# Kernel optimization log

Measured on AMD Instinct MI355X. Metric: run time of the kernel, lower is better.

## Reference

```python
import jax, jax.numpy as jnp
import numpy as np

# Config constants (match init_kwargs)
D_MODEL = 1024
N_EXPERTS = 8
EXPERT_SCALE = 2          # experts per base group -> n_base_groups = 4
N_FEAT = 16
BANK_DIM = 32
RAW_FEAT = N_FEAT * BANK_DIM   # 512
PROJ_DIM = 256
R_HIDDEN = 256
E_HIDDEN = 256
TOP_K = 2
TEMP = 1.0
LN_EPS = 1e-5


def _layernorm(x, g, b):
    mu = jnp.mean(x, axis=-1, keepdims=True)
    var = jnp.mean((x - mu) ** 2, axis=-1, keepdims=True)
    return (x - mu) * jax.lax.rsqrt(var + LN_EPS) * g + b


def _softmax_top_k(logits, k):
    # keep top-k logits, mask rest to -inf, softmax
    topv = jax.lax.top_k(logits, k)[0]
    thresh = topv[..., -1:]
    masked = jnp.where(logits >= thresh, logits, -jnp.inf)
    return jax.nn.softmax(masked, axis=-1)


def setup_inputs() -> dict:
    key = jax.random.key(0)
    ks = jax.random.split(key, 24)
    B, S = 4, 2048
    s = 0.02
    inp = {
        "hidden": jax.random.normal(ks[0], (B, S, D_MODEL), jnp.float32),
        "feat": jax.random.normal(ks[1], (B, S, N_FEAT), jnp.float32),
        "feat_bank": jax.random.normal(ks[2], (B, S, N_FEAT, BANK_DIM), jnp.float32),
        "item_seq_len": jax.random.randint(ks[3], (B,), 1, S + 1, jnp.int64),
        # pre-LN
        "ln_g": jnp.ones((D_MODEL,), jnp.float32),
        "ln_b": jnp.zeros((D_MODEL,), jnp.float32),
        # router feature projector (2 layers: Linear -> GELU -> Linear)
        "fp_w1": jax.random.normal(ks[4], (RAW_FEAT, PROJ_DIM), jnp.float32) * s,
        "fp_b1": jnp.zeros((PROJ_DIM,), jnp.float32),
        "fp_w2": jax.random.normal(ks[5], (PROJ_DIM, PROJ_DIM), jnp.float32) * s,
        "fp_b2": jnp.zeros((PROJ_DIM,), jnp.float32),
        # learned router MLP: d_in = d_model + proj_dim
        "r_w1": jax.random.normal(ks[6], (D_MODEL + PROJ_DIM, R_HIDDEN), jnp.float32) * s,
        "r_b1": jnp.zeros((R_HIDDEN,), jnp.float32),
        "r_w2": jax.random.normal(ks[7], (R_HIDDEN, N_EXPERTS), jnp.float32) * s,
        "r_b2": jnp.zeros((N_EXPERTS,), jnp.float32),
        # rule router (linear on raw stage features)
        "rr_w": jax.random.normal(ks[8], (N_FEAT, N_EXPERTS), jnp.float32) * s,
        "rr_b": jnp.zeros((N_EXPERTS,), jnp.float32),
        # per-expert FFN
        "e_w1": jax.random.normal(ks[9], (N_EXPERTS, D_MODEL, E_HIDDEN), jnp.float32) * s,
        "e_b1": jnp.zeros((N_EXPERTS, E_HIDDEN), jnp.float32),
        "e_w2": jax.random.normal(ks[10], (N_EXPERTS, E_HIDDEN, D_MODEL), jnp.float32) * s,
        "e_b2": jnp.zeros((N_EXPERTS, D_MODEL), jnp.float32),
        "alpha": jnp.ones((), jnp.float32),
    }
    return inp


def reference(hidden, feat, feat_bank, item_seq_len, ln_g, ln_b,
              fp_w1, fp_b1, fp_w2, fp_b2,
              r_w1, r_b1, r_w2, r_b2,
              rr_w, rr_b,
              e_w1, e_b1, e_w2, e_b2, alpha):
    B, S, D = hidden.shape
    h_norm = _layernorm(hidden, ln_g, ln_b)  # [B,S,D]

    # router feature path: flatten bank, 2-layer GELU projector
    bank_flat = feat_bank.reshape(B, S, RAW_FEAT)
    proj = jnp.dot(jax.nn.gelu(jnp.dot(bank_flat, fp_w1) + fp_b1), fp_w2) + fp_b2  # [B,S,P]

    # token-mode router input: concat hidden + projected features
    router_input = jnp.concatenate([h_norm, proj], axis=-1)
    rule_logits = jnp.dot(feat, rr_w) + rr_b  # rule router on raw stage features

    raw_logits = jnp.dot(jax.nn.gelu(jnp.dot(router_input, r_w1) + r_b1), r_w2) + r_b2
    scaled_logits = raw_logits / max(TEMP, 1e-6)
    gate_weights = _softmax_top_k(scaled_logits, TOP_K)           # [B,S,E]
    rule_target_logits = rule_logits / max(TEMP, 1e-6)

    # expert group: per-expert 2-layer GELU FFN on h_norm
    h1 = jax.nn.gelu(jnp.einsum('bsd,edh->bseh', h_norm, e_w1) + e_b1)
    expert_out = jnp.einsum('bseh,ehd->bsed', h1, e_w2) + e_b2    # [B,S,E,D]

    stage_out = jnp.einsum('bse,bsed->bsd', gate_weights, expert_out)
    next_hidden = hidden + alpha * stage_out

    # _aggregate_group_weights: expert_group_idx = arange(E)//EXPERT_SCALE is
    # contiguous, so gather+sum per group == reshape+sum over the scale axis
    n_groups = N_EXPERTS // EXPERT_SCALE
    group_weights = gate_weights.reshape(B, S, n_groups, EXPERT_SCALE).sum(-1)

    return (next_hidden, stage_out, gate_weights, scaled_logits, group_weights, rule_target_logits)
```

## Files before the change

### kernel.cpp

```cpp
#include <hip/hip_runtime.h>
#include <stdint.h>


typedef unsigned short u16;
using bf16x8 = __attribute__((ext_vector_type(8))) short;
using f32x4  = __attribute__((ext_vector_type(4))) float;

#define WS_HHI 0u
#define WS_HLO 16777216u
#define WS_PB2 33554432u
#define WS_W1T 67108864u
#define WS_IDX 71303168u
#define IX_SELE   0u
#define IX_SELG   65536u
#define IX_ROW    131072u
#define IX_TOKR   196608u
#define IX_GROW   262144u
#define IX_CNT    327680u
#define IX_CBASE  335872u
#define IX_TILEE  344064u
#define IX_TILES  344704u
#define IX_TILEC  345344u
#define IX_META   345984u
#define IX_TILEE2 346112u
#define IX_TILES2 347264u
#define IX_TILEC2 348416u

__device__ __forceinline__ float gelu_tanh(float x) {
  float x3 = x * x * x;
  float t = tanhf(0.7978845608028654f * (x + 0.044715f * x3));
  return 0.5f * x * (1.0f + t);
}
__device__ __forceinline__ u16 f2bf(float f) {
  uint32_t u = __float_as_uint(f);
  u = u + 0x7fffu + ((u >> 16) & 1u);
  return (u16)(u >> 16);
}
__device__ __forceinline__ float b2f(u16 h) {
  return __uint_as_float(((uint32_t)h) << 16);
}
__device__ __forceinline__ void gll16(const void* g, void* l) {
  __builtin_amdgcn_global_load_lds(
      (const __attribute__((address_space(1))) void*)g,
      (__attribute__((address_space(3))) void*)l, 16, 0, 0);
}

__global__ __launch_bounds__(256) void split_bank_kernel(const float* __restrict__ x,
    u16* __restrict__ hi, u16* __restrict__ lo) {
  int i4 = blockIdx.x * 256 + threadIdx.x;
  float4 v = ((const float4*)x)[i4];
  ushort4 h, l;
  h.x = f2bf(v.x); l.x = f2bf(v.x - b2f(h.x));
  h.y = f2bf(v.y); l.y = f2bf(v.y - b2f(h.y));
  h.z = f2bf(v.z); l.z = f2bf(v.z - b2f(h.z));
  h.w = f2bf(v.w); l.w = f2bf(v.w - b2f(h.w));
  ((ushort4*)hi)[i4] = h;
  ((ushort4*)lo)[i4] = l;
}

__global__ __launch_bounds__(256) void tsplit_kernel(const float* __restrict__ in,
    int inR, int inC, u16* __restrict__ outHi, u16* __restrict__ outLo,
    int outLD, int outColOff) {
  __shared__ u16 hs[64][65];
  __shared__ u16 ls[64][65];
  int tid = threadIdx.x;
  int c0 = blockIdx.x * 64, r0 = blockIdx.y * 64;
  const float* inp = in + (size_t)blockIdx.z * inR * inC;
  int rl = tid >> 6, cl = tid & 63;
#pragma unroll
  for (int p = 0; p < 16; p++) {
    int r = rl + p * 4;
    float v = inp[(size_t)(r0 + r) * inC + c0 + cl];
    u16 h = f2bf(v);
    hs[r][cl] = h;
    ls[r][cl] = f2bf(v - b2f(h));
  }
  __syncthreads();
  size_t obase = (size_t)(blockIdx.z * inC + c0) * outLD + outColOff + r0;
#pragma unroll
  for (int p = 0; p < 16; p++) {
    int c = rl + p * 4;
    outHi[obase + (size_t)c * outLD + cl] = hs[cl][c];
    if (outLo) outLo[obase + (size_t)c * outLD + cl] = ls[cl][c];
  }
}

__global__ __launch_bounds__(256) void wprime_kernel(const float* __restrict__ fp_w2,
    const float* __restrict__ r_w1, const float* __restrict__ fp_b2,
    const float* __restrict__ r_b1, float* __restrict__ wp, float* __restrict__ bp) {
  __shared__ float row[256];
  int i = blockIdx.x, n = threadIdx.x;
  if (i < 256) {
    row[n] = fp_w2[i * 256 + n];
    __syncthreads();
    float acc = 0.0f;
    for (int j = 0; j < 256; j++) acc += row[j] * r_w1[(size_t)(1024 + j) * 256 + n];
    wp[i * 256 + n] = acc;
  } else {
    row[n] = fp_b2[n];
    __syncthreads();
    float acc = r_b1[n];
    for (int j = 0; j < 256; j++) acc += row[j] * r_w1[(size_t)(1024 + j) * 256 + n];
    bp[n] = acc;
  }
}

__global__ __launch_bounds__(256) void ln_kernel(const float* __restrict__ hidden,
    const float* __restrict__ ln_g, const float* __restrict__ ln_b,
    const float* __restrict__ feat, const float* __restrict__ rr_w,
    const float* __restrict__ rr_b,
    u16* __restrict__ h_hi, u16* __restrict__ h_lo, float* __restrict__ rule) {
  int t = blockIdx.x;
  int tid = threadIdx.x;
  float4 v = ((const float4*)(hidden + (size_t)t * 1024))[tid];
  float s = v.x + v.y + v.z + v.w;
#pragma unroll
  for (int o = 32; o > 0; o >>= 1) s += __shfl_down(s, o);
  __shared__ float red[4];
  __shared__ float stats[2];
  int wid = tid >> 6, lane = tid & 63;
  if (lane == 0) red[wid] = s;
  __syncthreads();
  if (tid == 0) stats[0] = (red[0] + red[1] + red[2] + red[3]) * (1.0f / 1024.0f);
  __syncthreads();
  float mu = stats[0];
  float dx = v.x - mu, dy = v.y - mu, dz = v.z - mu, dw = v.w - mu;
  float q = dx * dx + dy * dy + dz * dz + dw * dw;
#pragma unroll
  for (int o = 32; o > 0; o >>= 1) q += __shfl_down(q, o);
  if (lane == 0) red[wid] = q;
  __syncthreads();
  if (tid == 0) {
    float var = (red[0] + red[1] + red[2] + red[3]) * (1.0f / 1024.0f) + 1e-5f;
    float r = rsqrtf(var);
    r = r * (1.5f - 0.5f * var * r * r);
    stats[1] = r;
  }
  __syncthreads();
  float r = stats[1];
  float4 g = ((const float4*)ln_g)[tid];
  float4 b = ((const float4*)ln_b)[tid];
  float4 o;
  o.x = dx * r * g.x + b.x;
  o.y = dy * r * g.y + b.y;
  o.z = dz * r * g.z + b.z;
  o.w = dw * r * g.w + b.w;
  ushort4 hv, lv;
  hv.x = f2bf(o.x); lv.x = f2bf(o.x - b2f(hv.x));
  hv.y = f2bf(o.y); lv.y = f2bf(o.y - b2f(hv.y));
  hv.z = f2bf(o.z); lv.z = f2bf(o.z - b2f(hv.z));
  hv.w = f2bf(o.w); lv.w = f2bf(o.w - b2f(hv.w));
  ((ushort4*)(h_hi + (size_t)t * 1024))[tid] = hv;
  ((ushort4*)(h_lo + (size_t)t * 1024))[tid] = lv;
  if (tid < 8) {
    float acc = rr_b[tid];
#pragma unroll
    for (int f = 0; f < 16; f++) acc += feat[t * 16 + f] * rr_w[f * 8 + tid];
    rule[t * 8 + tid] = acc;
  }
}

#define G3_STAGE(K, AH, AL, BH, BL)   \
  gll16(gAh0 + (K), AH + tid * 8);    \
  gll16(gAl0 + (K), AL + tid * 8);    \
  gll16(gBh0 + (K), BH + tid * 8);    \
  gll16(gBl0 + (K), BL + tid * 8);

#define G3_COMPUTE(AH, AL, BH, BL)                                             \
  {                                                                            \
    bf16x8 afh[2], afl[2], bfh[2], bfl[2];                                     \
    _Pragma("unroll") for (int i = 0; i < 2; i++) {                            \
      afh[i] = *((const bf16x8*)(AH + (wr + i * 16 + l16) * 32 + xq * 8));     \
      afl[i] = *((const bf16x8*)(AL + (wr + i * 16 + l16) * 32 + xq * 8));     \
      bfh[i] = *((const bf16x8*)(BH + (wc + i * 16 + l16) * 32 + xq * 8));     \
      bfl[i] = *((const bf16x8*)(BL + (wc + i * 16 + l16) * 32 + xq * 8));     \
    }                                                                          \
    _Pragma("unroll") for (int i = 0; i < 2; i++)                              \
      _Pragma("unroll") for (int j = 0; j < 2; j++) {                          \
        acc[i][j] = __builtin_amdgcn_mfma_f32_16x16x32_bf16(afh[i], bfh[j], acc[i][j], 0, 0, 0); \
        acc[i][j] = __builtin_amdgcn_mfma_f32_16x16x32_bf16(afl[i], bfh[j], acc[i][j], 0, 0, 0); \
        acc[i][j] = __builtin_amdgcn_mfma_f32_16x16x32_bf16(afh[i], bfl[j], acc[i][j], 0, 0, 0); \
      }                                                                        \
  }

__global__ __launch_bounds__(256) void gemm3_kernel(
    const u16* __restrict__ Ah, const u16* __restrict__ Al, int lda,
    int kchunk, int nz1,
    const u16* __restrict__ A2h, const u16* __restrict__ A2l, int lda2,
    int klen2, int bkoff2,
    const u16* __restrict__ Bth, const u16* __restrict__ Btl, int Kb,
    float* __restrict__ parts) {
  __shared__ u16 Ash0[2048], Ash1[2048];
  __shared__ u16 Asl0[2048], Asl1[2048];
  __shared__ u16 Bsh0[2048], Bsh1[2048];
  __shared__ u16 Bsl0[2048], Bsl1[2048];
  int tid = threadIdx.x;
  int z = blockIdx.z;
  const u16 *pAh, *pAl;
  int lda_, akoff, bkoff, klen;
  if (z < nz1) {
    pAh = Ah; pAl = Al; lda_ = lda; akoff = z * kchunk; bkoff = akoff; klen = kchunk;
  } else {
    pAh = A2h; pAl = A2l; lda_ = lda2; akoff = 0; bkoff = bkoff2; klen = klen2;
  }
  int row0 = blockIdx.y * 64, col0 = blockIdx.x * 64;
  int wave = tid >> 6, lane = tid & 63;
  int wr = (wave >> 1) * 32, wc = (wave & 1) * 32;
  int l16 = lane & 15, qd = lane >> 4;
  int xq = qd ^ ((l16 >> 1) & 3);
  f32x4 acc[2][2];
#pragma unroll
  for (int i = 0; i < 2; i++)
#pragma unroll
    for (int j = 0; j < 2; j++) acc[i][j] = 0.0f;

  int r0 = tid >> 2, kc = tid & 3;
  int kcs = kc ^ ((r0 >> 1) & 3);
  const u16* gAh0 = pAh + (size_t)(row0 + r0) * lda_ + akoff + kcs * 8;
  const u16* gAl0 = pAl + (size_t)(row0 + r0) * lda_ + akoff + kcs * 8;
  const u16* gBh0 = Bth + (size_t)(col0 + r0) * Kb + bkoff + kcs * 8;
  const u16* gBl0 = Btl + (size_t)(col0 + r0) * Kb + bkoff + kcs * 8;

  G3_STAGE(0, Ash0, Asl0, Bsh0, Bsl0);
  __syncthreads();
  for (int k0 = 0; k0 < klen; k0 += 64) {
    G3_STAGE(k0 + 32, Ash1, Asl1, Bsh1, Bsl1);
    G3_COMPUTE(Ash0, Asl0, Bsh0, Bsl0);
    __syncthreads();
    if (k0 + 64 < klen) {
      G3_STAGE(k0 + 64, Ash0, Asl0, Bsh0, Bsl0);
    }
    G3_COMPUTE(Ash1, Asl1, Bsh1, Bsl1);
    __syncthreads();
  }

  float* pz = parts + (size_t)z * 2097152;
#pragma unroll
  for (int i = 0; i < 2; i++)
#pragma unroll
    for (int j = 0; j < 2; j++) {
      int cl = wc + j * 16 + l16;
#pragma unroll
      for (int rr = 0; rr < 4; rr++) {
        int rl = wr + i * 16 + qd * 4 + rr;
        pz[(size_t)(row0 + rl) * 256 + col0 + cl] = acc[i][j][rr];
      }
    }
}

__global__ __launch_bounds__(256) void epi_bf_kernel(const float* __restrict__ parts,
    int nz, const float* __restrict__ bias, int do_gelu,
    u16* __restrict__ hi, u16* __restrict__ lo) {
  int i4 = blockIdx.x * 256 + threadIdx.x;
  float4 s = ((const float4*)parts)[i4];
  for (int zz = 1; zz < nz; zz++) {
    float4 p = ((const float4*)parts)[(size_t)zz * 524288 + i4];
    s.x += p.x; s.y += p.y; s.z += p.z; s.w += p.w;
  }
  float4 bv = ((const float4*)bias)[i4 & 63];
  s.x += bv.x; s.y += bv.y; s.z += bv.z; s.w += bv.w;
  if (do_gelu) {
    s.x = gelu_tanh(s.x); s.y = gelu_tanh(s.y);
    s.z = gelu_tanh(s.z); s.w = gelu_tanh(s.w);
  }
  ushort4 h, l;
  h.x = f2bf(s.x); l.x = f2bf(s.x - b2f(h.x));
  h.y = f2bf(s.y); l.y = f2bf(s.y - b2f(h.y));
  h.z = f2bf(s.z); l.z = f2bf(s.z - b2f(h.z));
  h.w = f2bf(s.w); l.w = f2bf(s.w - b2f(h.w));
  ((ushort4*)hi)[i4] = h;
  ((ushort4*)lo)[i4] = l;
}

__global__ __launch_bounds__(256) void epi_f32_kernel(const float* __restrict__ parts,
    int nz, const float* __restrict__ bias, float* __restrict__ out) {
  int i4 = blockIdx.x * 256 + threadIdx.x;
  float4 s = ((const float4*)parts)[i4];
  for (int zz = 1; zz < nz; zz++) {
    float4 p = ((const float4*)parts)[(size_t)zz * 524288 + i4];
    s.x += p.x; s.y += p.y; s.z += p.z; s.w += p.w;
  }
  float4 bv = ((const float4*)bias)[i4 & 63];
  s.x = gelu_tanh(s.x + bv.x);
  s.y = gelu_tanh(s.y + bv.y);
  s.z = gelu_tanh(s.z + bv.z);
  s.w = gelu_tanh(s.w + bv.w);
  ((float4*)out)[i4] = s;
}

__global__ __launch_bounds__(256) void gate_kernel(const float* __restrict__ r1,
    const float* __restrict__ r_w2, const float* __restrict__ r_b2,
    float* __restrict__ gates, float* __restrict__ slog, float* __restrict__ gw,
    int* __restrict__ selE, float* __restrict__ selG, int* __restrict__ cnt) {
  __shared__ float w2s[2048];
  __shared__ float r1s[32][260];
  __shared__ float lg[32][8];
  __shared__ int se_s[64];
  int tid = threadIdx.x;
  int blk = blockIdx.x;
  int t0 = blk * 32;
  for (int i = tid; i < 2048; i += 256) {
    int e = i >> 8, k = i & 255;
    w2s[i] = r_w2[k * 8 + e];
  }
  for (int i = tid; i < 8192; i += 256) {
    int tt = i >> 8, k = i & 255;
    r1s[tt][k] = r1[(size_t)(t0 + tt) * 256 + k];
  }
  __syncthreads();
  {
    int tl = tid >> 3, e = tid & 7;
    float acc = r_b2[e];
    const float* wrp = &w2s[e * 256];
    const float* rrp = &r1s[tl][0];
    for (int k = 0; k < 256; k += 4) {
      float4 a = *(const float4*)(rrp + k);
      float4 b = *(const float4*)(wrp + k);
      acc += a.x * b.x + a.y * b.y + a.z * b.z + a.w * b.w;
    }
    lg[tl][e] = acc;
  }
  __syncthreads();
  if (tid < 32) {
    int t = t0 + tid;
    float l[8];
#pragma unroll
    for (int i = 0; i < 8; i++) l[i] = lg[tid][i];
    float m1 = -1e30f, m2 = -1e30f;
    int i1 = 0, i2 = 0;
#pragma unroll
    for (int i = 0; i < 8; i++) {
      float v = l[i];
      if (v > m1) { m2 = m1; i2 = i1; m1 = v; i1 = i; }
      else if (v > m2) { m2 = v; i2 = i; }
    }
    float w[8];
    float se = 0.0f;
#pragma unroll
    for (int i = 0; i < 8; i++) {
      float ex = (l[i] >= m2) ? expf(l[i] - m1) : 0.0f;
      w[i] = ex;
      se += ex;
    }
    float inv = 1.0f / se;
#pragma unroll
    for (int i = 0; i < 8; i++) {
      gates[(size_t)t * 8 + i] = w[i] * inv;
      slog[(size_t)t * 8 + i] = l[i];
    }
#pragma unroll
    for (int gi = 0; gi < 4; gi++)
      gw[(size_t)t * 4 + gi] = (w[2 * gi] + w[2 * gi + 1]) * inv;
    se_s[tid * 2] = i1;
    se_s[tid * 2 + 1] = i2;
    selE[t * 2] = i1;      selG[t * 2] = w[i1] * inv;
    selE[t * 2 + 1] = i2;  selG[t * 2 + 1] = w[i2] * inv;
  }
  __syncthreads();
  if (tid < 8) {
    int c = 0;
#pragma unroll
    for (int s = 0; s < 64; s++) c += (se_s[s] == tid) ? 1 : 0;
    cnt[blk * 8 + tid] = c;
  }
}

__global__ __launch_bounds__(256) void stageb_kernel(const int* __restrict__ cnt,
    int* __restrict__ cbase, int* __restrict__ tileE, int* __restrict__ tileS,
    int* __restrict__ tileC, int* __restrict__ tileE2, int* __restrict__ tileS2,
    int* __restrict__ tileC2, int* __restrict__ meta) {
  __shared__ int cs[2048];
  __shared__ int tot[8];
  __shared__ int ebase[8];
  int tid = threadIdx.x;
  for (int i = tid; i < 2048; i += 256) cs[i] = cnt[i];
  __syncthreads();
  if (tid < 8) {
    int s = 0;
    for (int c = 0; c < 256; c++) s += cs[c * 8 + tid];
    tot[tid] = s;
  }
  __syncthreads();
  if (tid == 0) {
    int b = 0, nt = 0;
    for (int e = 0; e < 8; e++) {
      ebase[e] = b;
      int c = tot[e];
      for (int off = 0; off < c; off += 128) {
        tileE[nt] = e; tileS[nt] = b + off;
        tileC[nt] = (c - off < 128) ? (c - off) : 128;
        nt++;
      }
      b += c;
    }
    meta[16] = nt;
    int b2 = 0, nt2 = 0;
    for (int e = 0; e < 8; e++) {
      int c = tot[e];
      for (int off = 0; off < c; off += 64) {
        tileE2[nt2] = e; tileS2[nt2] = b2 + off;
        tileC2[nt2] = (c - off < 64) ? (c - off) : 64;
        nt2++;
      }
      b2 += c;
    }
    meta[17] = nt2;
  }
  __syncthreads();
  if (tid < 8) {
    int run = ebase[tid];
    for (int c = 0; c < 256; c++) {
      cbase[c * 8 + tid] = run;
      run += cs[c * 8 + tid];
    }
  }
}

__global__ __launch_bounds__(256) void scatter_kernel(const int* __restrict__ selE,
    const float* __restrict__ selG, const int* __restrict__ cbase,
    int* __restrict__ rowsel, int* __restrict__ tokrow, float* __restrict__ grow) {
  int chunk = blockIdx.x;
  int wave = threadIdx.x >> 6, lane = threadIdx.x & 63;
  int slot = chunk * 64 + lane;
  int sel = selE[slot];
  float g = selG[slot];
  int tokn = chunk * 32 + (lane >> 1);
  unsigned long long lt = (1ULL << lane) - 1ULL;
#pragma unroll
  for (int ei = 0; ei < 2; ei++) {
    int e = wave + ei * 4;
    unsigned long long m = __ballot(sel == e);
    if (sel == e) {
      int row = cbase[chunk * 8 + e] + __popcll(m & lt);
      rowsel[slot] = row;
      tokrow[row] = tokn;
      grow[row] = g;
    }
  }
}

__global__ __launch_bounds__(256) void gexp1_kernel(const u16* __restrict__ A,
    const u16* __restrict__ w1t, const float* __restrict__ e_b1,
    const int* __restrict__ tokrow, const float* __restrict__ grow,
    const int* __restrict__ tileE2, const int* __restrict__ tileS2,
    const int* __restrict__ tileC2, const int* __restrict__ meta,
    u16* __restrict__ pb1) {
  __shared__ u16 As0[64 * 32];
  __shared__ u16 As1[64 * 32];
  __shared__ u16 Bs0[64 * 32];
  __shared__ u16 Bs1[64 * 32];
  __shared__ float gsl[64];
  int n = blockIdx.x;
  int ty = ((n >> 5) << 3) + (n & 7);
  int cblk = (n >> 3) & 3;
  if (ty >= meta[17]) return;
  int e = tileE2[ty], pstart = tileS2[ty], pcnt = tileC2[ty];
  int tid = threadIdx.x;
  int col0 = cblk * 64;
  if (tid < 64) {
    int rr = (tid < pcnt) ? tid : (pcnt - 1);
    gsl[tid] = grow[pstart + rr];
  }
  int wave = tid >> 6, lane = tid & 63;
  int wr = (wave >> 1) * 32, wc = (wave & 1) * 32;
  int l16 = lane & 15, qd = lane >> 4;
  int xq = qd ^ ((l16 >> 1) & 3);
  f32x4 acc[2][2];
  acc[0][0] = 0.0f; acc[0][1] = 0.0f; acc[1][0] = 0.0f; acc[1][1] = 0.0f;

  int r0 = tid >> 2, kc = tid & 3;
  int kcs = kc ^ ((r0 >> 1) & 3);
  int ra = (r0 < pcnt) ? r0 : (pcnt - 1);
  int ta = tokrow[pstart + ra];
  const u16* Ap = A + (size_t)ta * 1024 + kcs * 8;
  const u16* Bp = w1t + (size_t)(e * 256 + col0 + r0) * 1024 + kcs * 8;
  u16* dA0 = As0 + tid * 8;
  u16* dA1 = As1 + tid * 8;
  u16* dB0 = Bs0 + tid * 8;
  u16* dB1 = Bs1 + tid * 8;

  int aoff0 = (wr + l16) * 32 + xq * 8;
  int aoff1 = aoff0 + 16 * 32;
  int boff0 = (wc + l16) * 32 + xq * 8;
  int boff1 = boff0 + 16 * 32;

  gll16(Ap, dA0);
  gll16(Bp, dB0);
  __syncthreads();

  for (int k0 = 0; k0 < 1024; k0 += 64) {
    {
      gll16(Ap + k0 + 32, dA1);
      gll16(Bp + k0 + 32, dB1);
      bf16x8 a0 = *((const bf16x8*)(As0 + aoff0));
      bf16x8 a1 = *((const bf16x8*)(As0 + aoff1));
      bf16x8 b0 = *((const bf16x8*)(Bs0 + boff0));
      bf16x8 b1 = *((const bf16x8*)(Bs0 + boff1));
      acc[0][0] = __builtin_amdgcn_mfma_f32_16x16x32_bf16(a0, b0, acc[0][0], 0, 0, 0);
      acc[0][1] = __builtin_amdgcn_mfma_f32_16x16x32_bf16(a0, b1, acc[0][1], 0, 0, 0);
      acc[1][0] = __builtin_amdgcn_mfma_f32_16x16x32_bf16(a1, b0, acc[1][0], 0, 0, 0);
      acc[1][1] = __builtin_amdgcn_mfma_f32_16x16x32_bf16(a1, b1, acc[1][1], 0, 0, 0);
      __syncthreads();
    }
    {
      if (k0 + 64 < 1024) {
        gll16(Ap + k0 + 64, dA0);
        gll16(Bp + k0 + 64, dB0);
      }
      bf16x8 a0 = *((const bf16x8*)(As1 + aoff0));
      bf16x8 a1 = *((const bf16x8*)(As1 + aoff1));
      bf16x8 b0 = *((const bf16x8*)(Bs1 + boff0));
      bf16x8 b1 = *((const bf16x8*)(Bs1 + boff1));
      acc[0][0] = __builtin_amdgcn_mfma_f32_16x16x32_bf16(a0, b0, acc[0][0], 0, 0, 0);
      acc[0][1] = __builtin_amdgcn_mfma_f32_16x16x32_bf16(a0, b1, acc[0][1], 0, 0, 0);
      acc[1][0] = __builtin_amdgcn_mfma_f32_16x16x32_bf16(a1, b0, acc[1][0], 0, 0, 0);
      acc[1][1] = __builtin_amdgcn_mfma_f32_16x16x32_bf16(a1, b1, acc[1][1], 0, 0, 0);
      __syncthreads();
    }
  }

#pragma unroll
  for (int i = 0; i < 2; i++)
#pragma unroll
    for (int j = 0; j < 2; j++) {
      int cl = wc + j * 16 + l16;
      int col = col0 + cl;
      float bc = e_b1[e * 256 + col];
#pragma unroll
      for (int rr = 0; rr < 4; rr++) {
        int rl = wr + i * 16 + qd * 4 + rr;
        if (rl < pcnt) {
          float v = gelu_tanh(acc[i][j][rr] + bc) * gsl[rl];
          pb1[(size_t)(pstart + rl) * 256 + col] = f2bf(v);
        }
      }
    }
}

#define GX2_STAGE(K, AS, BS)              \
  gll16(Ap0 + (K), AS + tid * 8);         \
  gll16(Ap1 + (K), AS + tid * 8 + 2048);  \
  gll16(Bp0 + (K), BS + tid * 8);         \
  gll16(Bp1 + (K), BS + tid * 8 + 2048);

#define GX2_COMPUTE(AS, BS)                                                   \
  {                                                                           \
    bf16x8 af[4], bfr[4];                                                     \
    _Pragma("unroll") for (int i = 0; i < 4; i++) {                           \
      af[i]  = *((const bf16x8*)(AS + (wr + i * 16 + l16) * 32 + xq * 8));    \
      bfr[i] = *((const bf16x8*)(BS + (wc + i * 16 + l16) * 32 + xq * 8));    \
    }                                                                         \
    _Pragma("unroll") for (int i = 0; i < 4; i++)                             \
      _Pragma("unroll") for (int j = 0; j < 4; j++)                           \
        acc[i][j] = __builtin_amdgcn_mfma_f32_16x16x32_bf16(af[i], bfr[j], acc[i][j], 0, 0, 0); \
  }

__global__ __launch_bounds__(256) void gexp2_kernel(const u16* __restrict__ pb1,
    const u16* __restrict__ w2te,
    const int* __restrict__ tileE, const int* __restrict__ tileS,
    const int* __restrict__ tileC, const int* __restrict__ meta,
    u16* __restrict__ pb2) {
  int ty = blockIdx.y;
  if (ty >= meta[16]) return;
  int e = tileE[ty], pstart = tileS[ty], pcnt = tileC[ty];
  if (pcnt <= 0) return;
  __shared__ u16 As0[4096], As1[4096];
  __shared__ u16 Bs0[4096], Bs1[4096];
  int tid = threadIdx.x;
  int col0 = blockIdx.x * 128;
  int wave = tid >> 6, lane = tid & 63;
  int wr = (wave >> 1) * 64, wc = (wave & 1) * 64;
  int l16 = lane & 15, qd = lane >> 4;
  int xq = qd ^ ((l16 >> 1) & 3);
  f32x4 acc[4][4];
#pragma unroll
  for (int i = 0; i < 4; i++)
#pragma unroll
    for (int j = 0; j < 4; j++) acc[i][j] = 0.0f;

  int r0 = tid >> 2, kc = tid & 3;
  int kcs = kc ^ ((r0 >> 1) & 3);
  int ra = (r0 < pcnt) ? r0 : (pcnt - 1);
  int rb = (r0 + 64 < pcnt) ? (r0 + 64) : (pcnt - 1);
  const u16* Ap0 = pb1 + (size_t)(pstart + ra) * 256 + kcs * 8;
  const u16* Ap1 = pb1 + (size_t)(pstart + rb) * 256 + kcs * 8;
  const u16* Bp0 = w2te + (size_t)(e * 1024 + col0 + r0) * 256 + kcs * 8;
  const u16* Bp1 = Bp0 + (size_t)64 * 256;

  GX2_STAGE(0, As0, Bs0);
  __syncthreads();
  for (int k0 = 0; k0 < 256; k0 += 64) {
    GX2_STAGE(k0 + 32, As1, Bs1);
    GX2_COMPUTE(As0, Bs0);
    __syncthreads();
    if (k0 + 64 < 256) {
      GX2_STAGE(k0 + 64, As0, Bs0);
    }
    GX2_COMPUTE(As1, Bs1);
    __syncthreads();
  }

#pragma unroll
  for (int i = 0; i < 4; i++)
#pragma unroll
    for (int j = 0; j < 4; j++) {
      int cl = wc + j * 16 + l16;
#pragma unroll
      for (int rr = 0; rr < 4; rr++) {
        int rl = wr + i * 16 + qd * 4 + rr;
        if (rl < pcnt)
          pb2[(size_t)(pstart + rl) * 1024 + col0 + cl] = f2bf(acc[i][j][rr]);
      }
    }
}

__global__ __launch_bounds__(256) void combine_kernel(const u16* __restrict__ pb2,
    const int* __restrict__ rowsel, const int* __restrict__ selE,
    const float* __restrict__ selG, const float* __restrict__ e_b2,
    const float* __restrict__ hidden, const float* __restrict__ alpha_p,
    float* __restrict__ stage, float* __restrict__ next) {
  int t = blockIdx.x;
  int c = threadIdx.x * 4;
  int rA = rowsel[t * 2], rB = rowsel[t * 2 + 1];
  int eA = selE[t * 2], eB = selE[t * 2 + 1];
  float gA = selG[t * 2], gB = selG[t * 2 + 1];
  float al = alpha_p[0];
  ushort4 pa = *((const ushort4*)(pb2 + (size_t)rA * 1024 + c));
  ushort4 pb = *((const ushort4*)(pb2 + (size_t)rB * 1024 + c));
  float4 ba = *((const float4*)(e_b2 + (size_t)eA * 1024 + c));
  float4 bb = *((const float4*)(e_b2 + (size_t)eB * 1024 + c));
  float4 h = *((const float4*)(hidden + (size_t)t * 1024 + c));
  float4 v;
  v.x = b2f(pa.x) + b2f(pb.x) + gA * ba.x + gB * bb.x;
  v.y = b2f(pa.y) + b2f(pb.y) + gA * ba.y + gB * bb.y;
  v.z = b2f(pa.z) + b2f(pb.z) + gA * ba.z + gB * bb.z;
  v.w = b2f(pa.w) + b2f(pb.w) + gA * ba.w + gB * bb.w;
  *((float4*)(stage + (size_t)t * 1024 + c)) = v;
  float4 n;
  n.x = h.x + al * v.x; n.y = h.y + al * v.y;
  n.z = h.z + al * v.z; n.w = h.w + al * v.w;
  *((float4*)(next + (size_t)t * 1024 + c)) = n;
}

extern "C" void kernel_launch(void* const* d_in, const int* in_sizes, int n_in,
                              void* d_out, int out_size, void* d_ws, size_t ws_size,
                              hipStream_t stream) {
  const float* hidden    = (const float*)d_in[0];
  const float* feat      = (const float*)d_in[1];
  const float* feat_bank = (const float*)d_in[2];
  const float* ln_g  = (const float*)d_in[4];
  const float* ln_b  = (const float*)d_in[5];
  const float* fp_w1 = (const float*)d_in[6];
  const float* fp_b1 = (const float*)d_in[7];
  const float* fp_w2 = (const float*)d_in[8];
  const float* fp_b2 = (const float*)d_in[9];
  const float* r_w1  = (const float*)d_in[10];
  const float* r_b1  = (const float*)d_in[11];
  const float* r_w2  = (const float*)d_in[12];
  const float* r_b2  = (const float*)d_in[13];
  const float* rr_w  = (const float*)d_in[14];
  const float* rr_b  = (const float*)d_in[15];
  const float* e_w1  = (const float*)d_in[16];
  const float* e_b1  = (const float*)d_in[17];
  const float* e_w2  = (const float*)d_in[18];
  const float* e_b2  = (const float*)d_in[19];
  const float* alpha = (const float*)d_in[20];

  char* ob = (char*)d_out;
  float* next  = (float*)ob;
  float* stage = (float*)(ob + 33554432);
  float* gates = (float*)(ob + 67108864);
  float* slog  = gates + 65536;
  float* gw    = slog + 65536;
  float* rule  = gw + 32768;

  u16* bank_hi  = (u16*)ob;
  u16* bank_lo  = (u16*)(ob + 8388608);
  float* r1     = (float*)ob;
  u16* fpw1t_hi = (u16*)(ob + 16777216);
  u16* fpw1t_lo = (u16*)(ob + 17039360);
  float* wp     = (float*)(ob + 17301504);
  float* bp     = (float*)(ob + 17563648);
  u16* rw1t_hi  = (u16*)(ob + 17825792);
  u16* rw1t_lo  = (u16*)(ob + 18481152);
  u16* mid_hi   = (u16*)(ob + 19136512);
  u16* mid_lo   = (u16*)(ob + 23330816);
  u16* w2te     = (u16*)(ob + 19136512);

  char* sb = ob + 33554432;
  float* parts = (float*)sb;
  u16* pb1     = (u16*)sb;

  char* ws = (char*)d_ws;
  u16* h_hi = (u16*)(ws + WS_HHI);
  u16* h_lo = (u16*)(ws + WS_HLO);
  u16* pb2  = (u16*)(ws + WS_PB2);
  u16* w1t  = (u16*)(ws + WS_W1T);
  char* ix  = ws + WS_IDX;
  int*   selE   = (int*)(ix + IX_SELE);
  float* selG   = (float*)(ix + IX_SELG);
  int*   rowsel = (int*)(ix + IX_ROW);
  int*   tokrow = (int*)(ix + IX_TOKR);
  float* grow   = (float*)(ix + IX_GROW);
  int*   cnt    = (int*)(ix + IX_CNT);
  int*   cbase  = (int*)(ix + IX_CBASE);
  int*   tileE  = (int*)(ix + IX_TILEE);
  int*   tileS  = (int*)(ix + IX_TILES);
  int*   tileC  = (int*)(ix + IX_TILEC);
  int*   tileE2 = (int*)(ix + IX_TILEE2);
  int*   tileS2 = (int*)(ix + IX_TILES2);
  int*   tileC2 = (int*)(ix + IX_TILEC2);
  int*   meta   = (int*)(ix + IX_META);

  split_bank_kernel<<<4096, 256, 0, stream>>>(feat_bank, bank_hi, bank_lo);
  wprime_kernel<<<257, 256, 0, stream>>>(fp_w2, r_w1, fp_b2, r_b1, wp, bp);
  tsplit_kernel<<<dim3(4, 8, 1), 256, 0, stream>>>(fp_w1, 512, 256,
      fpw1t_hi, fpw1t_lo, 512, 0);
  tsplit_kernel<<<dim3(4, 16, 1), 256, 0, stream>>>(r_w1, 1024, 256,
      rw1t_hi, rw1t_lo, 1280, 0);
  tsplit_kernel<<<dim3(4, 4, 1), 256, 0, stream>>>(wp, 256, 256,
      rw1t_hi, rw1t_lo, 1280, 1024);
  tsplit_kernel<<<dim3(4, 16, 8), 256, 0, stream>>>(e_w1, 1024, 256,
      w1t, nullptr, 1024, 0);
  ln_kernel<<<8192, 256, 0, stream>>>(hidden, ln_g, ln_b, feat, rr_w, rr_b,
                                      h_hi, h_lo, rule);
  gemm3_kernel<<<dim3(4, 128, 2), 256, 0, stream>>>(
      bank_hi, bank_lo, 512, 256, 2,
      bank_hi, bank_lo, 512, 0, 0,
      fpw1t_hi, fpw1t_lo, 512, parts);
  epi_bf_kernel<<<2048, 256, 0, stream>>>(parts, 2, fp_b1, 1, mid_hi, mid_lo);
  gemm3_kernel<<<dim3(4, 128, 3), 256, 0, stream>>>(
      h_hi, h_lo, 1024, 512, 2,
      mid_hi, mid_lo, 256, 256, 1024,
      rw1t_hi, rw1t_lo, 1280, parts);
  tsplit_kernel<<<dim3(16, 4, 8), 256, 0, stream>>>(e_w2, 256, 1024,
      w2te, nullptr, 256, 0);
  epi_f32_kernel<<<2048, 256, 0, stream>>>(parts, 3, bp, r1);
  gate_kernel<<<256, 256, 0, stream>>>(r1, r_w2, r_b2, gates, slog, gw,
      selE, selG, cnt);
  stageb_kernel<<<1, 256, 0, stream>>>(cnt, cbase, tileE, tileS, tileC,
      tileE2, tileS2, tileC2, meta);
  scatter_kernel<<<256, 256, 0, stream>>>(selE, selG, cbase, rowsel, tokrow, grow);
  gexp1_kernel<<<1152, 256, 0, stream>>>(h_hi, w1t, e_b1, tokrow, grow,
      tileE2, tileS2, tileC2, meta, pb1);
  gexp2_kernel<<<dim3(8, 136), 256, 0, stream>>>(pb1, w2te, tileE, tileS, tileC,
      meta, pb2);
  combine_kernel<<<8192, 256, 0, stream>>>(pb2, rowsel, selE, selG, e_b2,
      hidden, alpha, stage, next);
}
```

Measured before the change: 359.7 us.

## Fuse router GEMMs with bias-GELU epilogues and drop split-K partials

Replaces the split-K GEMM plus separate reduction/epilogue kernels with one kernel per router GEMM that walks the full K range (concatenating the two A sources) and applies bias, GELU and bf16 hi/lo split in-register. This removes the fp32 partial-sum round trip through global memory and two launches. Blocks are remapped so groups of row tiles share column tiles, which may help L2 reuse. In exchange the grid shrinks from 1024/1536 to 512 blocks with longer K loops, reducing parallelism, and the epilogue writes scalar rather than vectorized outputs.

Result: faster. 338.8 us (-5.8%).

```diff
diff --git a/kernel.cpp b/kernel.cpp
--- a/kernel.cpp
+++ b/kernel.cpp
@@ -160,13 +160,7 @@
   }
 }
 
-#define G3_STAGE(K, AH, AL, BH, BL)   \
-  gll16(gAh0 + (K), AH + tid * 8);    \
-  gll16(gAl0 + (K), AL + tid * 8);    \
-  gll16(gBh0 + (K), BH + tid * 8);    \
-  gll16(gBl0 + (K), BL + tid * 8);
-
-#define G3_COMPUTE(AH, AL, BH, BL)                                             \
+#define GF_COMPUTE(AH, AL, BH, BL)                                             \
   {                                                                            \
     bf16x8 afh[2], afl[2], bfh[2], bfl[2];                                     \
     _Pragma("unroll") for (int i = 0; i < 2; i++) {                            \
@@ -183,27 +177,21 @@
       }                                                                        \
   }
 
-__global__ __launch_bounds__(256) void gemm3_kernel(
-    const u16* __restrict__ Ah, const u16* __restrict__ Al, int lda,
-    int kchunk, int nz1,
-    const u16* __restrict__ A2h, const u16* __restrict__ A2l, int lda2,
-    int klen2, int bkoff2,
+__global__ __launch_bounds__(256) void gfuse_kernel(
+    const u16* __restrict__ A1h, const u16* __restrict__ A1l, int lda1, int klen1,
+    const u16* __restrict__ A2h, const u16* __restrict__ A2l, int lda2, int klen2,
     const u16* __restrict__ Bth, const u16* __restrict__ Btl, int Kb,
-    float* __restrict__ parts) {
+    const float* __restrict__ bias,
+    u16* __restrict__ outHi, u16* __restrict__ outLo, int fout) {
   __shared__ u16 Ash0[2048], Ash1[2048];
   __shared__ u16 Asl0[2048], Asl1[2048];
   __shared__ u16 Bsh0[2048], Bsh1[2048];
   __shared__ u16 Bsl0[2048], Bsl1[2048];
   int tid = threadIdx.x;
-  int z = blockIdx.z;
-  const u16 *pAh, *pAl;
-  int lda_, akoff, bkoff, klen;
-  if (z < nz1) {
-    pAh = Ah; pAl = Al; lda_ = lda; akoff = z * kchunk; bkoff = akoff; klen = kchunk;
-  } else {
-    pAh = A2h; pAl = A2l; lda_ = lda2; akoff = 0; bkoff = bkoff2; klen = klen2;
-  }
-  int row0 = blockIdx.y * 64, col0 = blockIdx.x * 64;
+  int n = blockIdx.x;
+  int rowt = ((n >> 5) << 3) + (n & 7);
+  int cblk = (n >> 3) & 3;
+  int row0 = rowt * 64, col0 = cblk * 64;
   int wave = tid >> 6, lane = tid & 63;
   int wr = (wave >> 1) * 32, wc = (wave & 1) * 32;
   int l16 = lane & 15, qd = lane >> 4;
@@ -215,77 +203,75 @@
     for (int j = 0; j < 2; j++) acc[i][j] = 0.0f;
 
   int r0 = tid >> 2, kc = tid & 3;
-  int kcs = kc ^ ((r0 >> 1) & 3);
-  const u16* gAh0 = pAh + (size_t)(row0 + r0) * lda_ + akoff + kcs * 8;
-  const u16* gAl0 = pAl + (size_t)(row0 + r0) * lda_ + akoff + kcs * 8;
-  const u16* gBh0 = Bth + (size_t)(col0 + r0) * Kb + bkoff + kcs * 8;
-  const u16* gBl0 = Btl + (size_t)(col0 + r0) * Kb + bkoff + kcs * 8;
-
-  G3_STAGE(0, Ash0, Asl0, Bsh0, Bsl0);
-  __syncthreads();
-  for (int k0 = 0; k0 < klen; k0 += 64) {
-    G3_STAGE(k0 + 32, Ash1, Asl1, Bsh1, Bsl1);
-    G3_COMPUTE(Ash0, Asl0, Bsh0, Bsl0);
+  int kcs8 = (kc ^ ((r0 >> 1) & 3)) * 8;
+  const u16* A1hp = A1h + (size_t)(row0 + r0) * lda1 + kcs8;
+  const u16* A1lp = A1l + (size_t)(row0 + r0) * lda1 + kcs8;
+  const u16* A2hp = A2h ? A2h + (size_t)(row0 + r0) * lda2 + kcs8 : (const u16*)0;
+  const u16* A2lp = A2l ? A2l + (size_t)(row0 + r0) * lda2 + kcs8 : (const u16*)0;
+  const u16* Bhp = Bth + (size_t)(col0 + r0) * Kb + kcs8;
+  const u16* Blp = Btl + (size_t)(col0 + r0) * Kb + kcs8;
+  int KT = klen1 + klen2;
+
+#define GF_STAGE(K, AH, AL, BH, BL)                       \
+  {                                                       \
+    int kk = (K);                                         \
+    if (kk < klen1) {                                     \
+      gll16(A1hp + kk, AH + tid * 8);                     \
+      gll16(A1lp + kk, AL + tid * 8);                     \
+    } else {                                              \
+      gll16(A2hp + (kk - klen1), AH + tid * 8);           \
+      gll16(A2lp + (kk - klen1), AL + tid * 8);           \
+    }                                                     \
+    gll16(Bhp + kk, BH + tid * 8);                        \
+    gll16(Blp + kk, BL + tid * 8);                        \
+  }
+
+  GF_STAGE(0, Ash0, Asl0, Bsh0, Bsl0);
+  __syncthreads();
+  for (int k0 = 0; k0 < KT; k0 += 64) {
+    GF_STAGE(k0 + 32, Ash1, Asl1, Bsh1, Bsl1);
+    GF_COMPUTE(Ash0, Asl0, Bsh0, Bsl0);
     __syncthreads();
-    if (k0 + 64 < klen) {
-      G3_STAGE(k0 + 64, Ash0, Asl0, Bsh0, Bsl0);
-    }
-    G3_COMPUTE(Ash1, Asl1, Bsh1, Bsl1);
+    if (k0 + 64 < KT) {
+      GF_STAGE(k0 + 64, Ash0, Asl0, Bsh0, Bsl0);
+    }
+    GF_COMPUTE(Ash1, Asl1, Bsh1, Bsl1);
     __syncthreads();
   }
-
-  float* pz = parts + (size_t)z * 2097152;
-#pragma unroll
-  for (int i = 0; i < 2; i++)
-#pragma unroll
-    for (int j = 0; j < 2; j++) {
-      int cl = wc + j * 16 + l16;
-#pragma unroll
-      for (int rr = 0; rr < 4; rr++) {
-        int rl = wr + i * 16 + qd * 4 + rr;
-        pz[(size_t)(row0 + rl) * 256 + col0 + cl] = acc[i][j][rr];
+#undef GF_STAGE
+
+  if (fout) {
+    float* of = (float*)outHi;
+#pragma unroll
+    for (int i = 0; i < 2; i++)
+#pragma unroll
+      for (int j = 0; j < 2; j++) {
+        int cl = wc + j * 16 + l16;
+        float bc = bias[col0 + cl];
+#pragma unroll
+        for (int rr = 0; rr < 4; rr++) {
+          int rl = wr + i * 16 + qd * 4 + rr;
+          of[(size_t)(row0 + rl) * 256 + col0 + cl] = gelu_tanh(acc[i][j][rr] + bc);
+        }
       }
-    }
-}
-
-__global__ __launch_bounds__(256) void epi_bf_kernel(const float* __restrict__ parts,
-    int nz, const float* __restrict__ bias, int do_gelu,
-    u16* __restrict__ hi, u16* __restrict__ lo) {
-  int i4 = blockIdx.x * 256 + threadIdx.x;
-  float4 s = ((const float4*)parts)[i4];
-  for (int zz = 1; zz < nz; zz++) {
-    float4 p = ((const float4*)parts)[(size_t)zz * 524288 + i4];
-    s.x += p.x; s.y += p.y; s.z += p.z; s.w += p.w;
-  }
-  float4 bv = ((const float4*)bias)[i4 & 63];
-  s.x += bv.x; s.y += bv.y; s.z += bv.z; s.w += bv.w;
-  if (do_gelu) {
-    s.x = gelu_tanh(s.x); s.y = gelu_tanh(s.y);
-    s.z = gelu_tanh(s.z); s.w = gelu_tanh(s.w);
-  }
-  ushort4 h, l;
-  h.x = f2bf(s.x); l.x = f2bf(s.x - b2f(h.x));
-  h.y = f2bf(s.y); l.y = f2bf(s.y - b2f(h.y));
-  h.z = f2bf(s.z); l.z = f2bf(s.z - b2f(h.z));
-  h.w = f2bf(s.w); l.w = f2bf(s.w - b2f(h.w));
-  ((ushort4*)hi)[i4] = h;
-  ((ushort4*)lo)[i4] = l;
-}
-
-__global__ __launch_bounds__(256) void epi_f32_kernel(const float* __restrict__ parts,
-    int nz, const float* __restrict__ bias, float* __restrict__ out) {
-  int i4 = blockIdx.x * 256 + threadIdx.x;
-  float4 s = ((const float4*)parts)[i4];
-  for (int zz = 1; zz < nz; zz++) {
-    float4 p = ((const float4*)parts)[(size_t)zz * 524288 + i4];
-    s.x += p.x; s.y += p.y; s.z += p.z; s.w += p.w;
-  }
-  float4 bv = ((const float4*)bias)[i4 & 63];
-  s.x = gelu_tanh(s.x + bv.x);
-  s.y = gelu_tanh(s.y + bv.y);
-  s.z = gelu_tanh(s.z + bv.z);
-  s.w = gelu_tanh(s.w + bv.w);
-  ((float4*)out)[i4] = s;
+  } else {
+#pragma unroll
+    for (int i = 0; i < 2; i++)
+#pragma unroll
+      for (int j = 0; j < 2; j++) {
+        int cl = wc + j * 16 + l16;
+        float bc = bias[col0 + cl];
+#pragma unroll
+        for (int rr = 0; rr < 4; rr++) {
+          int rl = wr + i * 16 + qd * 4 + rr;
+          float v = gelu_tanh(acc[i][j][rr] + bc);
+          u16 h = f2bf(v);
+          size_t o = (size_t)(row0 + rl) * 256 + col0 + cl;
+          outHi[o] = h;
+          outLo[o] = f2bf(v - b2f(h));
+        }
+      }
+  }
 }
 
 __global__ __launch_bounds__(256) void gate_kernel(const float* __restrict__ r1,
@@ -688,7 +674,6 @@
   u16* w2te     = (u16*)(ob + 19136512);
 
   char* sb = ob + 33554432;
-  float* parts = (float*)sb;
   u16* pb1     = (u16*)sb;
 
   char* ws = (char*)d_ws;
@@ -724,18 +709,16 @@
       w1t, nullptr, 1024, 0);
   ln_kernel<<<8192, 256, 0, stream>>>(hidden, ln_g, ln_b, feat, rr_w, rr_b,
                                       h_hi, h_lo, rule);
-  gemm3_kernel<<<dim3(4, 128, 2), 256, 0, stream>>>(
-      bank_hi, bank_lo, 512, 256, 2,
-      bank_hi, bank_lo, 512, 0, 0,
-      fpw1t_hi, fpw1t_lo, 512, parts);
-  epi_bf_kernel<<<2048, 256, 0, stream>>>(parts, 2, fp_b1, 1, mid_hi, mid_lo);
-  gemm3_kernel<<<dim3(4, 128, 3), 256, 0, stream>>>(
-      h_hi, h_lo, 1024, 512, 2,
-      mid_hi, mid_lo, 256, 256, 1024,
-      rw1t_hi, rw1t_lo, 1280, parts);
+  gfuse_kernel<<<512, 256, 0, stream>>>(
+      bank_hi, bank_lo, 512, 512,
+      nullptr, nullptr, 0, 0,
+      fpw1t_hi, fpw1t_lo, 512, fp_b1, mid_hi, mid_lo, 0);
+  gfuse_kernel<<<512, 256, 0, stream>>>(
+      h_hi, h_lo, 1024, 1024,
+      mid_hi, mid_lo, 256, 256,
+      rw1t_hi, rw1t_lo, 1280, bp, (u16*)r1, nullptr, 1);
   tsplit_kernel<<<dim3(16, 4, 8), 256, 0, stream>>>(e_w2, 256, 1024,
       w2te, nullptr, 256, 0);
-  epi_f32_kernel<<<2048, 256, 0, stream>>>(parts, 3, bp, r1);
   gate_kernel<<<256, 256, 0, stream>>>(r1, r_w2, r_b2, gates, slog, gw,
       selE, selG, cnt);
   stageb_kernel<<<1, 256, 0, stream>>>(cnt, cbase, tileE, tileS, tileC,
```
